# Performance work log

Measured on AMD Instinct MI355X. Metric: run time of the kernel, lower is better.

The kernel has to match this reference:

```python
import jax, jax.numpy as jnp
import numpy as np

HEAD_NUM = 4
B, S, D = 8, 1024, 512


def setup_inputs() -> dict:
    k = jax.random.key(0)
    kq, kk, kv = jax.random.split(k, 3)
    return {
        "query": jax.random.normal(kq, (B, S, D), dtype=jnp.float32),
        "key": jax.random.normal(kk, (B, S, D), dtype=jnp.float32),
        "value": jax.random.normal(kv, (B, S, D), dtype=jnp.float32),
    }


def _corr_attention(q, k, v):
    # q,k,v: [B, H, S, hd]
    score = jnp.einsum('bhqd,bhkd->bhqk', q, k)  # raw dot products
    len_q = jnp.sqrt(jnp.sum(q * q, axis=-1))    # [B,H,S]
    len_k = jnp.sqrt(jnp.sum(k * k, axis=-1))    # [B,H,S]
    score = score / (len_q[..., :, None] * len_k[..., None, :])  # cosine similarity
    signal = jnp.sign(score)
    flat = jnp.abs(score).reshape(-1)            # global flatten across B,H,S,S
    n = flat.shape[0]
    idx = jnp.argsort(-flat)                     # descending sort indices
    prob = (jnp.arange(n, dtype=flat.dtype) + 1.0) / n  # (1/n, 2/n, ..., 1)
    ranked = flat.at[idx].set(prob)              # rank-transform: largest -> smallest prob
    score = (-jnp.log(ranked)).reshape(signal.shape) * signal
    return jnp.einsum('bhqk,bhkd->bhqd', score, v)


def reference(query, key, value):
    b, s, d = query.shape
    h = HEAD_NUM
    q = query.reshape(b, s, h, -1).transpose(0, 2, 1, 3)
    k = key.reshape(b, s, h, -1).transpose(0, 2, 1, 3)
    v = value.reshape(b, s, h, -1).transpose(0, 2, 1, 3)
    out = _corr_attention(q, k, v)               # [B,H,S,hd]
    return out.transpose(0, 2, 1, 3).reshape(b, s, d)
```

## Files before the change

kernel.cpp:

```cpp
#include <hip/hip_runtime.h>
#include <math.h>

#define BB 8
#define SS 1024
#define DD 512
#define HH 4
#define HD 128
#define N_SC (BB*HH*SS*SS)

#define NB 8192
#define BINS 13107.2f
#define NBLK 2048
#define NP2 32

#define OFF_QN    0
#define SZ_QN     ((size_t)BB*SS*DD*2)
#define OFF_KN    (OFF_QN + SZ_QN)
#define OFF_VT    (OFF_KN + SZ_QN)
#define OFF_PARTS (OFF_VT + SZ_QN)
#define SZ_PARTS  ((size_t)NBLK*(NB/4)*4)
#define OFF_WMAG  (OFF_PARTS + SZ_PARTS)
#define OFF_PART2 (OFF_WMAG + (size_t)NB*2)

typedef __bf16 bf16x8 __attribute__((ext_vector_type(8)));
typedef float  f32x4  __attribute__((ext_vector_type(4)));
typedef unsigned short ushort_t;

__device__ __forceinline__ unsigned bf16rne(float x) {
  unsigned b = __float_as_uint(x);
  return (b + 0x7FFFu + ((b >> 16) & 1u)) >> 16;
}
__device__ __forceinline__ unsigned sbin(float s) {
  return (unsigned)fminf(fabsf(s)*BINS, 8191.0f);
}

__global__ __launch_bounds__(256) void prep_vt_kernel(
    const float* __restrict__ q, const float* __restrict__ k,
    const float* __restrict__ v,
    unsigned* __restrict__ qn, unsigned* __restrict__ kn,
    unsigned* __restrict__ vt) {
  __shared__ float T[64][65];
  int t = threadIdx.x;
  if (blockIdx.x < 16384) {
    int lane = t & 63;
    int row = blockIdx.x*4 + (t >> 6);
    const float* src; unsigned* dst; int r;
    if (row < 32768) { src = q; dst = qn; r = row; }
    else             { src = k; dst = kn; r = row - 32768; }
    int b = r >> 12, s = (r >> 2) & 1023, h = r & 3;
    float2 vv = *(const float2*)(src + ((size_t)(b*1024 + s))*512 + h*128 + lane*2);
    float sum = vv.x*vv.x + vv.y*vv.y;
    #pragma unroll
    for (int off = 32; off; off >>= 1) sum += __shfl_xor(sum, off, 64);
    float inv = rsqrtf(sum);
    unsigned u = bf16rne(vv.x*inv) | (bf16rne(vv.y*inv) << 16);
    dst[(size_t)((b*4 + h)*1024 + s)*64 + lane] = u;
  } else {
    int vb = blockIdx.x - 16384;
    int s0 = (vb & 15)*64, d0 = ((vb >> 4) & 1)*64, bh = vb >> 5;
    int b = bh >> 2, h = bh & 3;
    #pragma unroll
    for (int i = 0; i < 16; i++) {
      int idx = t + i*256, rs = idx >> 6, cd = idx & 63;
      T[rs][cd] = v[((size_t)(b*1024 + s0 + rs))*512 + h*128 + d0 + cd];
    }
    __syncthreads();
    #pragma unroll
    for (int i = 0; i < 8; i++) {
      int idx = t + i*256, rd = idx >> 5, c2 = (idx & 31)*2;
      unsigned u = bf16rne(T[c2][rd]) | (bf16rne(T[c2+1][rd]) << 16);
      vt[(size_t)(bh*128 + d0 + rd)*512 + (s0 + c2)/2] = u;
    }
  }
}

__global__ __launch_bounds__(256) void scores_hist_kernel(
    const ushort_t* __restrict__ qn, const ushort_t* __restrict__ kn,
    unsigned* __restrict__ parts) {
  __shared__ ushort_t Qs[128*128];
  __shared__ ushort_t Ks[128*128];
  __shared__ unsigned h8[NB/4];
  int t = threadIdx.x;
  int bh = blockIdx.z, sq0 = blockIdx.y*128, sk0 = blockIdx.x*128;

  #pragma unroll
  for (int i = 0; i < 8; i++) h8[t + i*256] = 0;

  const uint4* qg = (const uint4*)qn + (size_t)(bh*1024 + sq0)*16;
  const uint4* kg = (const uint4*)kn + (size_t)(bh*1024 + sk0)*16;
  #pragma unroll
  for (int i = 0; i < 8; i++) {
    int idx = t + i*256, row = idx >> 4, g = idx & 15;
    int sw = g ^ (row & 15);
    *(uint4*)&Qs[row*128 + sw*8] = qg[row*16 + g];
    *(uint4*)&Ks[row*128 + sw*8] = kg[row*16 + g];
  }
  __syncthreads();

  int w = t >> 6, lane = t & 63, m16 = lane & 15, q2 = lane >> 4;
  int wm = (w >> 1)*64, wn = (w & 1)*64;
  f32x4 acc[4][4];
  #pragma unroll
  for (int i = 0; i < 4; i++)
    #pragma unroll
    for (int j = 0; j < 4; j++) acc[i][j] = (f32x4){0.f,0.f,0.f,0.f};

  #pragma unroll
  for (int ks = 0; ks < 4; ks++) {
    int sw = ((ks*4 + q2) ^ m16)*8;
    bf16x8 a[4], bb[4];
    #pragma unroll
    for (int i = 0; i < 4; i++) a[i]  = *(const bf16x8*)&Qs[(wm + i*16 + m16)*128 + sw];
    #pragma unroll
    for (int j = 0; j < 4; j++) bb[j] = *(const bf16x8*)&Ks[(wn + j*16 + m16)*128 + sw];
    #pragma unroll
    for (int i = 0; i < 4; i++)
      #pragma unroll
      for (int j = 0; j < 4; j++)
        acc[i][j] = __builtin_amdgcn_mfma_f32_16x16x32_bf16(a[i], bb[j], acc[i][j], 0, 0, 0);
  }

  #pragma unroll
  for (int i = 0; i < 4; i++)
    #pragma unroll
    for (int j = 0; j < 4; j++)
      #pragma unroll
      for (int p = 0; p < 4; p++) {
        unsigned bin = sbin(acc[i][j][p]);
        atomicAdd(&h8[bin >> 2], 1u << ((bin & 3)*8));
      }
  __syncthreads();

  int blockId = (bh*64) + blockIdx.y*8 + blockIdx.x;
  unsigned* dst = parts + (size_t)blockId*(NB/4);
  #pragma unroll
  for (int i = 0; i < 8; i++) dst[t + i*256] = h8[t + i*256];
}

__global__ __launch_bounds__(256) void reduce1_kernel(
    const unsigned* __restrict__ parts, unsigned* __restrict__ parts2) {
  int g = blockIdx.x*256 + threadIdx.x;
  int p0 = blockIdx.y*64;
  unsigned s0 = 0, s1 = 0, s2 = 0, s3 = 0;
  #pragma unroll 8
  for (int p = p0; p < p0 + 64; p++) {
    unsigned w = parts[(size_t)p*(NB/4) + g];
    s0 += w & 0xFFu; s1 += (w >> 8) & 0xFFu;
    s2 += (w >> 16) & 0xFFu; s3 += w >> 24;
  }
  uint4 o = {s0, s1, s2, s3};
  ((uint4*)parts2)[(size_t)blockIdx.y*(NB/4) + g] = o;
}

__global__ __launch_bounds__(1024) void scan_kernel(
    const unsigned* __restrict__ parts2, ushort_t* __restrict__ wmag) {
  __shared__ unsigned d[1024];
  int t = threadIdx.x;
  unsigned loc[8] = {0,0,0,0,0,0,0,0};
  #pragma unroll 4
  for (int p = 0; p < NP2; p++) {
    uint4 a = ((const uint4*)parts2)[(size_t)p*(NB/4) + t*2];
    uint4 b2 = ((const uint4*)parts2)[(size_t)p*(NB/4) + t*2 + 1];
    loc[0] += a.x;  loc[1] += a.y;  loc[2] += a.z;  loc[3] += a.w;
    loc[4] += b2.x; loc[5] += b2.y; loc[6] += b2.z; loc[7] += b2.w;
  }
  unsigned tot = 0;
  #pragma unroll
  for (int j = 0; j < 8; j++) tot += loc[j];
  d[t] = tot; __syncthreads();
  for (int off = 1; off < 1024; off <<= 1) {
    unsigned x = (t >= off) ? d[t - off] : 0u;
    __syncthreads();
    d[t] += x;
    __syncthreads();
  }
  unsigned run = d[t] - tot;
  const float inv_n = 1.0f / (float)N_SC;
  #pragma unroll
  for (int j = 0; j < 8; j++) {
    run += loc[j];
    float rm = (float)(N_SC - run) + 0.5f*(float)(loc[j] + 1u);
    wmag[t*8 + j] = (ushort_t)bf16rne(-logf(rm * inv_n));
  }
}

__global__ __launch_bounds__(256) void out_kernel(
    const ushort_t* __restrict__ qn, const ushort_t* __restrict__ kn,
    const ushort_t* __restrict__ wmag, const ushort_t* __restrict__ vt,
    float* __restrict__ out) {
  __shared__ ushort_t Qs[64*128];
  __shared__ ushort_t Ks[128*128];
  __shared__ ushort_t Ws[64*128];
  __shared__ ushort_t Wl[NB];
  int t = threadIdx.x;
  int bh = blockIdx.y, q0 = blockIdx.x*64;
  int b = bh >> 2, h = bh & 3;

  #pragma unroll
  for (int i = 0; i < 4; i++)
    ((uint4*)Wl)[t + i*256] = ((const uint4*)wmag)[t + i*256];

  const uint4* qg = (const uint4*)qn + (size_t)(bh*1024 + q0)*16;
  #pragma unroll
  for (int i = 0; i < 4; i++) {
    int idx = t + i*256, row = idx >> 4, g = idx & 15;
    *(uint4*)&Qs[row*128 + (g ^ (row & 15))*8] = qg[row*16 + g];
  }

  int w = t >> 6, lane = t & 63, m16 = lane & 15, q2 = lane >> 4;
  int wq = (w >> 1)*32, wd = (w & 1)*64;
  f32x4 oacc[2][4];
  #pragma unroll
  for (int i = 0; i < 2; i++)
    #pragma unroll
    for (int j = 0; j < 4; j++) oacc[i][j] = (f32x4){0.f,0.f,0.f,0.f};

  for (int kc = 0; kc < 8; kc++) {
    const uint4* kg = (const uint4*)kn + (size_t)(bh*1024 + kc*128)*16;
    #pragma unroll
    for (int i = 0; i < 8; i++) {
      int idx = t + i*256, row = idx >> 4, g = idx & 15;
      *(uint4*)&Ks[row*128 + (g ^ (row & 15))*8] = kg[row*16 + g];
    }
    __syncthreads();

    f32x4 sacc[2][4];
    #pragma unroll
    for (int i = 0; i < 2; i++)
      #pragma unroll
      for (int j = 0; j < 4; j++) sacc[i][j] = (f32x4){0.f,0.f,0.f,0.f};
    #pragma unroll
    for (int ks = 0; ks < 4; ks++) {
      int sw = ((ks*4 + q2) ^ m16)*8;
      bf16x8 a[2], bb[4];
      #pragma unroll
      for (int i = 0; i < 2; i++) a[i]  = *(const bf16x8*)&Qs[(wq + i*16 + m16)*128 + sw];
      #pragma unroll
      for (int j = 0; j < 4; j++) bb[j] = *(const bf16x8*)&Ks[(wd + j*16 + m16)*128 + sw];
      #pragma unroll
      for (int i = 0; i < 2; i++)
        #pragma unroll
        for (int j = 0; j < 4; j++)
          sacc[i][j] = __builtin_amdgcn_mfma_f32_16x16x32_bf16(a[i], bb[j], sacc[i][j], 0, 0, 0);
    }
    __syncthreads();

    #pragma unroll
    for (int i = 0; i < 2; i++)
      #pragma unroll
      for (int j = 0; j < 4; j++)
        #pragma unroll
        for (int p = 0; p < 4; p++) {
          float s = sacc[i][j][p];
          unsigned wm = (s == 0.f) ? 0u
                        : (unsigned)Wl[sbin(s)] | ((s < 0.f) ? 0x8000u : 0u);
          int row = wq + i*16 + q2*4 + p;
          int col = wd + j*16 + m16;
          Ws[row*128 + ((col >> 3) ^ (row & 15))*8 + (col & 7)] = (ushort_t)wm;
        }
    __syncthreads();

    const uint4* vg = (const uint4*)vt;
    #pragma unroll
    for (int ks = 0; ks < 4; ks++) {
      int sw = ((ks*4 + q2) ^ m16)*8;
      bf16x8 a[2], bb[4];
      #pragma unroll
      for (int i = 0; i < 2; i++) a[i] = *(const bf16x8*)&Ws[(wq + i*16 + m16)*128 + sw];
      #pragma unroll
      for (int j = 0; j < 4; j++)
        bb[j] = *(const bf16x8*)&vg[(size_t)(bh*128 + wd + j*16 + m16)*128 + kc*16 + ks*4 + q2];
      #pragma unroll
      for (int i = 0; i < 2; i++)
        #pragma unroll
        for (int j = 0; j < 4; j++)
          oacc[i][j] = __builtin_amdgcn_mfma_f32_16x16x32_bf16(a[i], bb[j], oacc[i][j], 0, 0, 0);
    }
  }

  #pragma unroll
  for (int i = 0; i < 2; i++)
    #pragma unroll
    for (int p = 0; p < 4; p++) {
      int qrow = q0 + wq + i*16 + q2*4 + p;
      #pragma unroll
      for (int j = 0; j < 4; j++) {
        int dcol = wd + j*16 + m16;
        out[(size_t)(b*1024 + qrow)*512 + h*128 + dcol] = oacc[i][j][p];
      }
    }
}

extern "C" void kernel_launch(void* const* d_in, const int* in_sizes, int n_in,
                              void* d_out, int out_size, void* d_ws, size_t ws_size,
                              hipStream_t stream) {
  const float* q = (const float*)d_in[0];
  const float* k = (const float*)d_in[1];
  const float* v = (const float*)d_in[2];
  float* out = (float*)d_out;
  char* ws = (char*)d_ws;

  unsigned* qn    = (unsigned*)(ws + OFF_QN);
  unsigned* kn    = (unsigned*)(ws + OFF_KN);
  unsigned* vtb   = (unsigned*)(ws + OFF_VT);
  unsigned* parts = (unsigned*)(ws + OFF_PARTS);
  ushort_t* wmag  = (ushort_t*)(ws + OFF_WMAG);
  unsigned* part2 = (unsigned*)(ws + OFF_PART2);

  hipLaunchKernelGGL(prep_vt_kernel, dim3(17408), dim3(256), 0, stream, q, k, v, qn, kn, vtb);
  hipLaunchKernelGGL(scores_hist_kernel, dim3(8, 8, 32), dim3(256), 0, stream,
                     (const ushort_t*)qn, (const ushort_t*)kn, parts);
  hipLaunchKernelGGL(reduce1_kernel, dim3(8, NP2), dim3(256), 0, stream, parts, part2);
  hipLaunchKernelGGL(scan_kernel, dim3(1), dim3(1024), 0, stream, part2, wmag);
  hipLaunchKernelGGL(out_kernel, dim3(16, 32), dim3(256), 0, stream,
                     (const ushort_t*)qn, (const ushort_t*)kn, wmag,
                     (const ushort_t*)vtb, out);
}
```

Baseline: 191.3 us.

## Prefetch K and V into registers in out_kernel and remap block indices

The out_kernel now loads the next K chunk into registers during the score and weight phase, then writes it to shared memory after the PV MFMAs. This replaces the blocking load and barrier at the top of each iteration. V fragments for the current chunk are issued at loop start so their global latency overlaps the QK MFMAs. Both the histogram and output kernels switch to a 1D grid with bh in the low bits, which changes the order in which blocks are scheduled across CUs and caches. The prefetch adds register pressure (kreg plus 16 uint4 of vreg), which can reduce occupancy.

```diff
diff --git a/kernel.cpp b/kernel.cpp
--- a/kernel.cpp
+++ b/kernel.cpp
@@ -81,7 +81,9 @@
   __shared__ ushort_t Ks[128*128];
   __shared__ unsigned h8[NB/4];
   int t = threadIdx.x;
-  int bh = blockIdx.z, sq0 = blockIdx.y*128, sk0 = blockIdx.x*128;
+  int L = blockIdx.x;
+  int bh = L & 31, tile = L >> 5;
+  int sq0 = (tile >> 3)*128, sk0 = (tile & 7)*128;
 
   #pragma unroll
   for (int i = 0; i < 8; i++) h8[t + i*256] = 0;
@@ -131,8 +133,7 @@
       }
   __syncthreads();
 
-  int blockId = (bh*64) + blockIdx.y*8 + blockIdx.x;
-  unsigned* dst = parts + (size_t)blockId*(NB/4);
+  unsigned* dst = parts + (size_t)L*(NB/4);
   #pragma unroll
   for (int i = 0; i < 8; i++) dst[t + i*256] = h8[t + i*256];
 }
@@ -193,7 +194,8 @@
   __shared__ ushort_t Ws[64*128];
   __shared__ ushort_t Wl[NB];
   int t = threadIdx.x;
-  int bh = blockIdx.y, q0 = blockIdx.x*64;
+  int L = blockIdx.x;
+  int bh = L & 31, q0 = (L >> 5)*64;
   int b = bh >> 2, h = bh & 3;
 
   #pragma unroll
@@ -207,6 +209,23 @@
     *(uint4*)&Qs[row*128 + (g ^ (row & 15))*8] = qg[row*16 + g];
   }
 
+  int srow = t >> 1, sg8 = (t & 1)*8;
+  (void)srow; (void)sg8;
+  uint4 kreg[8];
+  {
+    const uint4* kg = (const uint4*)kn + (size_t)(bh*1024)*16;
+    #pragma unroll
+    for (int i = 0; i < 8; i++) {
+      int idx = t + i*256, row = idx >> 4, g = idx & 15;
+      kreg[i] = kg[row*16 + g];
+    }
+    #pragma unroll
+    for (int i = 0; i < 8; i++) {
+      int idx = t + i*256, row = idx >> 4, g = idx & 15;
+      *(uint4*)&Ks[row*128 + (g ^ (row & 15))*8] = kreg[i];
+    }
+  }
+
   int w = t >> 6, lane = t & 63, m16 = lane & 15, q2 = lane >> 4;
   int wq = (w >> 1)*32, wd = (w & 1)*64;
   f32x4 oacc[2][4];
@@ -215,14 +234,16 @@
     #pragma unroll
     for (int j = 0; j < 4; j++) oacc[i][j] = (f32x4){0.f,0.f,0.f,0.f};
 
+  const uint4* vg = (const uint4*)vt;
   for (int kc = 0; kc < 8; kc++) {
-    const uint4* kg = (const uint4*)kn + (size_t)(bh*1024 + kc*128)*16;
-    #pragma unroll
-    for (int i = 0; i < 8; i++) {
-      int idx = t + i*256, row = idx >> 4, g = idx & 15;
-      *(uint4*)&Ks[row*128 + (g ^ (row & 15))*8] = kg[row*16 + g];
-    }
-    __syncthreads();
+    __syncthreads();
+
+    uint4 vreg[16];
+    #pragma unroll
+    for (int ks = 0; ks < 4; ks++)
+      #pragma unroll
+      for (int j = 0; j < 4; j++)
+        vreg[ks*4+j] = vg[(size_t)(bh*128 + wd + j*16 + m16)*128 + kc*16 + ks*4 + q2];
 
     f32x4 sacc[2][4];
     #pragma unroll
@@ -243,7 +264,16 @@
         for (int j = 0; j < 4; j++)
           sacc[i][j] = __builtin_amdgcn_mfma_f32_16x16x32_bf16(a[i], bb[j], sacc[i][j], 0, 0, 0);
     }
-    __syncthreads();
+
+    int kc2 = (kc < 7) ? kc + 1 : 7;
+    {
+      const uint4* kg = (const uint4*)kn + (size_t)(bh*1024 + kc2*128)*16;
+      #pragma unroll
+      for (int i = 0; i < 8; i++) {
+        int idx = t + i*256, row = idx >> 4, g = idx & 15;
+        kreg[i] = kg[row*16 + g];
+      }
+    }
 
     #pragma unroll
     for (int i = 0; i < 2; i++)
@@ -260,21 +290,24 @@
         }
     __syncthreads();
 
-    const uint4* vg = (const uint4*)vt;
     #pragma unroll
     for (int ks = 0; ks < 4; ks++) {
       int sw = ((ks*4 + q2) ^ m16)*8;
-      bf16x8 a[2], bb[4];
+      bf16x8 a[2];
       #pragma unroll
       for (int i = 0; i < 2; i++) a[i] = *(const bf16x8*)&Ws[(wq + i*16 + m16)*128 + sw];
-      #pragma unroll
-      for (int j = 0; j < 4; j++)
-        bb[j] = *(const bf16x8*)&vg[(size_t)(bh*128 + wd + j*16 + m16)*128 + kc*16 + ks*4 + q2];
       #pragma unroll
       for (int i = 0; i < 2; i++)
         #pragma unroll
         for (int j = 0; j < 4; j++)
-          oacc[i][j] = __builtin_amdgcn_mfma_f32_16x16x32_bf16(a[i], bb[j], oacc[i][j], 0, 0, 0);
+          oacc[i][j] = __builtin_amdgcn_mfma_f32_16x16x32_bf16(
+              a[i], *(const bf16x8*)&vreg[ks*4+j], oacc[i][j], 0, 0, 0);
+    }
+
+    #pragma unroll
+    for (int i = 0; i < 8; i++) {
+      int idx = t + i*256, row = idx >> 4, g = idx & 15;
+      *(uint4*)&Ks[row*128 + (g ^ (row & 15))*8] = kreg[i];
     }
   }
 
@@ -308,11 +341,11 @@
   unsigned* part2 = (unsigned*)(ws + OFF_PART2);
 
   hipLaunchKernelGGL(prep_vt_kernel, dim3(17408), dim3(256), 0, stream, q, k, v, qn, kn, vtb);
-  hipLaunchKernelGGL(scores_hist_kernel, dim3(8, 8, 32), dim3(256), 0, stream,
+  hipLaunchKernelGGL(scores_hist_kernel, dim3(NBLK), dim3(256), 0, stream,
                      (const ushort_t*)qn, (const ushort_t*)kn, parts);
   hipLaunchKernelGGL(reduce1_kernel, dim3(8, NP2), dim3(256), 0, stream, parts, part2);
   hipLaunchKernelGGL(scan_kernel, dim3(1), dim3(1024), 0, stream, part2, wmag);
-  hipLaunchKernelGGL(out_kernel, dim3(16, 32), dim3(256), 0, stream,
+  hipLaunchKernelGGL(out_kernel, dim3(512), dim3(256), 0, stream,
                      (const ushort_t*)qn, (const ushort_t*)kn, wmag,
                      (const ushort_t*)vtb, out);
 }
```

Measured after the change: 257.1 us. 1.34x slower.
